# Performance work log

Hardware: AMD Instinct MI355X
Metric: run time of the kernel (lower is better)

## Reference

```python
import jax, jax.numpy as jnp
import numpy as np

N_NODES = 100000
N_EDGES = 1000000
N_GRAPHS = 64
NODE_IN = 4
HID = 64
SIG = 16
NEG_SLOPE = 0.2


def _gat_layer(x, src, dst, W, a_src, a_dst, bias, n_nodes, concat):
    # W: [H*D, F_in], a_src/a_dst: [H, D], bias: [H*D] or [D]
    H, D = a_src.shape
    h = (x @ W.T).reshape(-1, H, D)                      # [N, H, D]
    alpha_src = jnp.sum(h * a_src[None], axis=-1)        # [N, H]
    alpha_dst = jnp.sum(h * a_dst[None], axis=-1)        # [N, H]
    e = alpha_src[src] + alpha_dst[dst]                  # [E, H]
    e = jax.nn.leaky_relu(e, NEG_SLOPE)
    # segment softmax over edges grouped by destination node
    e_max = jax.ops.segment_max(e, dst, num_segments=n_nodes)   # [N, H]
    e_exp = jnp.exp(e - e_max[dst])                              # [E, H]
    denom = jax.ops.segment_sum(e_exp, dst, num_segments=n_nodes)
    alpha = e_exp / denom[dst]                                   # [E, H]
    out = jax.ops.segment_sum(alpha[:, :, None] * h[src], dst, num_segments=n_nodes)  # [N,H,D]
    if concat:
        out = out.reshape(-1, H * D)
    else:
        out = out.mean(axis=1)
    return out + bias


def setup_inputs() -> dict:
    key = jax.random.key(0)
    ks = jax.random.split(key, 16)
    x = jax.random.normal(ks[0], (N_NODES, NODE_IN), dtype=jnp.float32)
    edge_index = jax.random.randint(ks[1], (2, N_EDGES), 0, N_NODES, dtype=jnp.int32)
    batch = jnp.sort(jax.random.randint(ks[2], (N_NODES,), 0, N_GRAPHS, dtype=jnp.int32))
    s = 0.1
    # conv1: heads=2, concat -> out 128
    w1 = jax.random.normal(ks[3], (2 * HID, NODE_IN), dtype=jnp.float32) * s
    att_src1 = jax.random.normal(ks[4], (2, HID), dtype=jnp.float32) * s
    att_dst1 = jax.random.normal(ks[5], (2, HID), dtype=jnp.float32) * s
    b1 = jnp.zeros((2 * HID,), dtype=jnp.float32)
    # conv2: heads=1, mean -> out 64
    w2 = jax.random.normal(ks[6], (HID, 2 * HID), dtype=jnp.float32) * s
    att_src2 = jax.random.normal(ks[7], (1, HID), dtype=jnp.float32) * s
    att_dst2 = jax.random.normal(ks[8], (1, HID), dtype=jnp.float32) * s
    b2 = jnp.zeros((HID,), dtype=jnp.float32)
    wp = jax.random.normal(ks[9], (SIG, HID), dtype=jnp.float32) * s
    bp = jnp.zeros((SIG,), dtype=jnp.float32)
    return {"x": x, "edge_index": edge_index, "batch": batch,
            "w1": w1, "att_src1": att_src1, "att_dst1": att_dst1, "b1": b1,
            "w2": w2, "att_src2": att_src2, "att_dst2": att_dst2, "b2": b2,
            "wp": wp, "bp": bp}


def reference(x, edge_index, batch, w1, att_src1, att_dst1, b1,
              w2, att_src2, att_dst2, b2, wp, bp):
    n = x.shape[0]
    loops = jnp.arange(n, dtype=edge_index.dtype)
    src = jnp.concatenate([edge_index[0], loops])  # PyG GATConv adds self-loops
    dst = jnp.concatenate([edge_index[1], loops])
    h = jax.nn.elu(_gat_layer(x, src, dst, w1, att_src1, att_dst1, b1, n, concat=True))
    h = jax.nn.elu(_gat_layer(h, src, dst, w2, att_src2, att_dst2, b2, n, concat=False))
    # global mean pool by graph id
    sums = jax.ops.segment_sum(h, batch, num_segments=N_GRAPHS)
    cnts = jax.ops.segment_sum(jnp.ones((n,), h.dtype), batch, num_segments=N_GRAPHS)
    pooled = sums / jnp.maximum(cnts, 1.0)[:, None]
    return (pooled @ wp.T + bp).squeeze()
```

## Files before the change

### kernel.cpp

```cpp
#include <hip/hip_runtime.h>
#include <hip/hip_fp16.h>

#define N_NODES  100000
#define N_EDGES  1000000
#define E_TOT    1100000
#define E_CAP    1500000
#define N_GRAPHS 64

typedef _Float16 half8 __attribute__((ext_vector_type(8)));
typedef float    f32x4 __attribute__((ext_vector_type(4)));

__device__ __forceinline__ float elu_f(float v) {
    return v > 0.f ? v : expm1f(v);
}

__device__ __forceinline__ float lrelu(float v) {
    return v > 0.f ? v : 0.2f * v;
}

__global__ void k_pre(const float* __restrict__ w1,
                      const float* __restrict__ as1v, const float* __restrict__ ad1v,
                      const float* __restrict__ w2,
                      const float* __restrict__ as2v, const float* __restrict__ ad2v,
                      float* __restrict__ A1, float* __restrict__ D1,
                      float* __restrict__ B2, float* __restrict__ E2)
{
    int t = threadIdx.x;
    if (t < 128) {
        float acc = 0.f;
        for (int d = 0; d < 64; ++d) acc += w2[d * 128 + t] * as2v[d];
        B2[t] = acc;
    } else {
        int k = t - 128;
        float acc = 0.f;
        for (int d = 0; d < 64; ++d) acc += w2[d * 128 + k] * ad2v[d];
        E2[k] = acc;
    }
    if (t < 8) {
        int h = t >> 2, k = t & 3;
        float acc = 0.f;
        for (int d = 0; d < 64; ++d) acc += w1[(h * 64 + d) * 4 + k] * as1v[h * 64 + d];
        A1[t] = acc;
    } else if (t < 16) {
        int i = t - 8, h = i >> 2, k = i & 3;
        float acc = 0.f;
        for (int d = 0; d < 64; ++d) acc += w1[(h * 64 + d) * 4 + k] * ad1v[h * 64 + d];
        D1[i] = acc;
    }
}

__global__ void k_pre2(const float* __restrict__ w2, __half* __restrict__ w2frag)
{
    int f = blockIdx.x * 256 + threadIdx.x;
    int j = f & 7, ln = (f >> 3) & 63, g = f >> 9;
    int nt = g >> 2, ks = g & 3;
    int col = nt * 16 + (ln & 15);
    int k   = ks * 32 + ((ln >> 4) << 3) + j;
    w2frag[f] = __float2half(w2[col * 128 + k]);
}

__global__ void k_count(const int* __restrict__ ei, int* __restrict__ deg, int* __restrict__ pos)
{
    int e = blockIdx.x * blockDim.x + threadIdx.x;
    if (e >= E_TOT) return;
    int dst = (e < N_EDGES) ? ei[N_EDGES + e] : (e - N_EDGES);
    pos[e] = atomicAdd(&deg[dst], 1);
}

__global__ void k_scan1(const int* __restrict__ deg, int* __restrict__ rowptr, int* __restrict__ bsum)
{
    __shared__ int sh[256];
    int tid = threadIdx.x;
    int i = blockIdx.x * 256 + tid;
    int v = (i <= N_NODES) ? ((deg[i] + 3) & ~3) : 0;
    int acc = v;
    sh[tid] = acc; __syncthreads();
    for (int off = 1; off < 256; off <<= 1) {
        int add = (tid >= off) ? sh[tid - off] : 0;
        __syncthreads();
        acc += add;
        sh[tid] = acc;
        __syncthreads();
    }
    if (i <= N_NODES) rowptr[i] = acc - v;
    if (tid == 255) bsum[blockIdx.x] = acc;
}

__global__ void k_scan2(int* __restrict__ bsum, int nb)
{
    __shared__ int sh[512];
    int tid = threadIdx.x;
    int v = (tid < nb) ? bsum[tid] : 0;
    int acc = v;
    sh[tid] = acc; __syncthreads();
    for (int off = 1; off < 512; off <<= 1) {
        int add = (tid >= off) ? sh[tid - off] : 0;
        __syncthreads();
        acc += add;
        sh[tid] = acc;
        __syncthreads();
    }
    if (tid < nb) bsum[tid] = acc - v;
}

__global__ void k_scan3(int* __restrict__ rowptr, const int* __restrict__ bsum)
{
    int i = blockIdx.x * 256 + threadIdx.x;
    if (i <= N_NODES) rowptr[i] += bsum[blockIdx.x];
}

__global__ void k_scatter(const int* __restrict__ ei, const int* __restrict__ rowptr,
                          const int* __restrict__ pos, int* __restrict__ srcs)
{
    int e = blockIdx.x * blockDim.x + threadIdx.x;
    if (e >= E_TOT) return;
    int src = (e < N_EDGES) ? ei[e] : (e - N_EDGES);
    int dst = (e < N_EDGES) ? ei[N_EDGES + e] : (e - N_EDGES);
    srcs[rowptr[dst] + pos[e]] = src;
}

__global__ void __launch_bounds__(256) k_gather1x(
    const int* __restrict__ srcs, const int* __restrict__ rowptr, const int* __restrict__ deg,
    const float* __restrict__ x,
    const float* __restrict__ A1c, const float* __restrict__ D1c,
    float4* __restrict__ agg0, float4* __restrict__ agg1, float2* __restrict__ wsA)
{
    const int tid  = threadIdx.x;
    const int n    = blockIdx.x * 16 + (tid >> 4);
    const int lane = tid & 15;
    if (n >= N_NODES) return;

    const float4 A0 = ((const float4*)A1c)[0], A1v = ((const float4*)A1c)[1];
    const float4 D0 = ((const float4*)D1c)[0], D1v = ((const float4*)D1c)[1];
    const float4 xn = ((const float4*)x)[n];
    const float ad0 = xn.x * D0.x + xn.y * D0.y + xn.z * D0.z + xn.w * D0.w;
    const float ad1 = xn.x * D1v.x + xn.y * D1v.y + xn.z * D1v.z + xn.w * D1v.w;

    const int beg = rowptr[n], rend = beg + deg[n];
    float4 acc0 = {0.f, 0.f, 0.f, 0.f}, acc1 = {0.f, 0.f, 0.f, 0.f};
    float ws0 = 0.f, ws1 = 0.f;
    for (int j = beg + lane; j < rend; j += 16) {
        const int s = srcs[j];
        const float4 xs = ((const float4*)x)[s];
        const float as0 = xs.x * A0.x + xs.y * A0.y + xs.z * A0.z + xs.w * A0.w;
        const float as1 = xs.x * A1v.x + xs.y * A1v.y + xs.z * A1v.z + xs.w * A1v.w;
        const float w0 = __expf(lrelu(as0 + ad0));
        const float w1 = __expf(lrelu(as1 + ad1));
        acc0.x = fmaf(w0, xs.x, acc0.x); acc0.y = fmaf(w0, xs.y, acc0.y);
        acc0.z = fmaf(w0, xs.z, acc0.z); acc0.w = fmaf(w0, xs.w, acc0.w);
        acc1.x = fmaf(w1, xs.x, acc1.x); acc1.y = fmaf(w1, xs.y, acc1.y);
        acc1.z = fmaf(w1, xs.z, acc1.z); acc1.w = fmaf(w1, xs.w, acc1.w);
        ws0 += w0; ws1 += w1;
    }
    #pragma unroll
    for (int off = 1; off < 16; off <<= 1) {
        acc0.x += __shfl_xor(acc0.x, off, 64);
        acc0.y += __shfl_xor(acc0.y, off, 64);
        acc0.z += __shfl_xor(acc0.z, off, 64);
        acc0.w += __shfl_xor(acc0.w, off, 64);
        acc1.x += __shfl_xor(acc1.x, off, 64);
        acc1.y += __shfl_xor(acc1.y, off, 64);
        acc1.z += __shfl_xor(acc1.z, off, 64);
        acc1.w += __shfl_xor(acc1.w, off, 64);
        ws0    += __shfl_xor(ws0,    off, 64);
        ws1    += __shfl_xor(ws1,    off, 64);
    }
    if (lane == 0) {
        agg0[n] = acc0;
        agg1[n] = acc1;
        wsA[n]  = make_float2(ws0, ws1);
    }
}

#define H2_NPB 64
#define SROW_H_LD 136
__global__ void __launch_bounds__(256) k_h2f(
    const float4* __restrict__ agg0, const float4* __restrict__ agg1,
    const float2* __restrict__ wsA,
    const float* __restrict__ w1, const float* __restrict__ b1,
    const __half* __restrict__ w2frag,
    const float* __restrict__ B2, const float* __restrict__ E2,
    __half* __restrict__ h2h, float* __restrict__ as2, float* __restrict__ ad2)
{
    __shared__ __align__(16) _Float16 srow[H2_NPB * SROW_H_LD];
    const int tid = threadIdx.x;
    const int bn  = blockIdx.x * H2_NPB;

    #pragma unroll 4
    for (int t = 0; t < 16; ++t) {
        int i = tid + t * 256;
        int r = i >> 6, c2 = i & 63;
        int n = bn + r;
        int head = c2 >> 5;
        float4 a; float ws;
        if (n < N_NODES) {
            a = head ? agg1[n] : agg0[n];
            float2 w = wsA[n];
            ws = head ? w.y : w.x;
        } else { a = make_float4(0.f, 0.f, 0.f, 0.f); ws = 1.f; }
        const float4 wA = ((const float4*)w1)[2 * c2];
        const float4 wB = ((const float4*)w1)[2 * c2 + 1];
        const float2 bb = ((const float2*)b1)[c2];
        float inv = 1.f / ws;
        float v0 = elu_f((a.x * wA.x + a.y * wA.y + a.z * wA.z + a.w * wA.w) * inv + bb.x);
        float v1 = elu_f((a.x * wB.x + a.y * wB.y + a.z * wB.z + a.w * wB.w) * inv + bb.y);
        *(__half2*)&srow[r * SROW_H_LD + 2 * c2] = __floats2half2_rn(v0, v1);
    }
    __syncthreads();

    {
        int r = tid >> 2, q = tid & 3;
        const __half2* row = (const __half2*)&srow[r * SROW_H_LD];
        float ps = 0.f, pd = 0.f;
        #pragma unroll 4
        for (int i = 0; i < 16; ++i) {
            int c2 = q * 16 + i;
            float2 v  = __half22float2(row[c2]);
            float2 Bv = ((const float2*)B2)[c2];
            float2 Ev = ((const float2*)E2)[c2];
            ps += v.x * Bv.x + v.y * Bv.y;
            pd += v.x * Ev.x + v.y * Ev.y;
        }
        ps += __shfl_xor(ps, 1, 64); ps += __shfl_xor(ps, 2, 64);
        pd += __shfl_xor(pd, 1, 64); pd += __shfl_xor(pd, 2, 64);
        int n = bn + r;
        if (q == 0 && n < N_NODES) { as2[n] = ps; ad2[n] = pd; }
    }

    const int lane = tid & 63;
    const int wv   = tid >> 6;
    const int mrow = lane & 15;
    const int kc   = lane >> 4;
    f32x4 acc[4] = {{0.f,0.f,0.f,0.f},{0.f,0.f,0.f,0.f},{0.f,0.f,0.f,0.f},{0.f,0.f,0.f,0.f}};
    const half8* __restrict__ wf = (const half8*)w2frag;
    #pragma unroll
    for (int ks = 0; ks < 4; ++ks) {
        const half8 af = *(const half8*)&srow[(wv * 16 + mrow) * SROW_H_LD + ks * 32 + kc * 8];
        #pragma unroll
        for (int nt = 0; nt < 4; ++nt) {
            const half8 bf = wf[(nt * 4 + ks) * 64 + lane];
            acc[nt] = __builtin_amdgcn_mfma_f32_16x16x32_f16(af, bf, acc[nt], 0, 0, 0);
        }
    }
    #pragma unroll
    for (int nt = 0; nt < 4; ++nt) {
        #pragma unroll
        for (int reg = 0; reg < 4; ++reg) {
            int node = bn + wv * 16 + ((lane >> 4) << 2) + reg;
            int dim  = nt * 16 + (lane & 15);
            if (node < N_NODES) h2h[(size_t)node * 64 + dim] = __float2half(acc[nt][reg]);
        }
    }
}

__global__ void __launch_bounds__(256) k_weights2(
    const int* __restrict__ rowptr, const int* __restrict__ deg, int* __restrict__ srcs,
    const float* __restrict__ as2, const float* __restrict__ ad2,
    float* __restrict__ w0p)
{
    int n = blockIdx.x * 16 + (threadIdx.x >> 4);
    int lane = threadIdx.x & 15;
    if (n >= N_NODES) return;
    int beg = rowptr[n], pend = rowptr[n + 1], rend = beg + deg[n];
    float adv = ad2[n];
    for (int j = beg + lane; j < pend; j += 16) {
        if (j < rend) {
            w0p[j] = __expf(lrelu(as2[srcs[j]] + adv));
        } else {
            srcs[j] = 0;
            w0p[j] = 0.f;
        }
    }
}

__global__ void __launch_bounds__(256) k_gather2(
    const int* __restrict__ srcs, const int* __restrict__ rowptr,
    const float* __restrict__ wcsr, const __half2* __restrict__ h2v,
    const float* __restrict__ b2, float* __restrict__ out2)
{
    const int tid  = threadIdx.x;
    const int n    = blockIdx.x * 4 + (tid >> 6);
    const int lane = tid & 63;
    const int eh   = lane >> 5;
    const int d2   = lane & 31;
    if (n >= N_NODES) return;
    const int beg = rowptr[n], end = rowptr[n + 1];

    float2 acc = {0.f, 0.f};
    float wsum = 0.f;
    for (int j = beg; j < end; j += 4) {
        const int4   s4 = *(const int4*)(srcs + j);
        const float4 w4 = *(const float4*)(wcsr + j);
        const int   sA = eh ? s4.z : s4.x;
        const int   sB = eh ? s4.w : s4.y;
        const float wA = eh ? w4.z : w4.x;
        const float wB = eh ? w4.w : w4.y;
        const float2 vA = __half22float2(h2v[(size_t)sA * 32 + d2]);
        const float2 vB = __half22float2(h2v[(size_t)sB * 32 + d2]);
        acc.x = fmaf(wA, vA.x, acc.x); acc.y = fmaf(wA, vA.y, acc.y);
        acc.x = fmaf(wB, vB.x, acc.x); acc.y = fmaf(wB, vB.y, acc.y);
        wsum += wA + wB;
    }
    acc.x += __shfl_xor(acc.x, 32, 64);
    acc.y += __shfl_xor(acc.y, 32, 64);
    wsum  += __shfl_xor(wsum,  32, 64);
    if (eh == 0) {
        const float2 bb = ((const float2*)b2)[d2];
        float2 o;
        o.x = elu_f(acc.x / wsum + bb.x);
        o.y = elu_f(acc.y / wsum + bb.y);
        ((float2*)out2)[(size_t)n * 32 + d2] = o;
    }
}

__global__ void __launch_bounds__(256) k_pool(
    const float* __restrict__ out2, const int* __restrict__ batch,
    float* __restrict__ pool, float* __restrict__ cnt)
{
    const int wv = threadIdx.x >> 6, d = threadIdx.x & 63;
    const int wid = blockIdx.x * 4 + wv;
    const int per = (N_NODES + 2047) / 2048;
    int n0 = wid * per, n1 = min(n0 + per, N_NODES);
    if (n0 >= n1) return;
    float acc = 0.f; int g = batch[n0]; int run = 0;
    for (int n = n0; n < n1; ++n) {
        int gn = batch[n];
        if (gn != g) {
            atomicAdd(&pool[g * 64 + d], acc);
            if (d == 0) atomicAdd(&cnt[g], (float)run);
            acc = 0.f; run = 0; g = gn;
        }
        acc += out2[(size_t)n * 64 + d];
        ++run;
    }
    atomicAdd(&pool[g * 64 + d], acc);
    if (d == 0) atomicAdd(&cnt[g], (float)run);
}

__global__ void k_head(const float* __restrict__ pool, const float* __restrict__ cnt,
                       const float* __restrict__ wp, const float* __restrict__ bp,
                       float* __restrict__ out)
{
    int t = threadIdx.x;
    int g = t >> 4, s = t & 15;
    float c = cnt[g]; if (c < 1.f) c = 1.f;
    float acc = bp[s];
    for (int d = 0; d < 64; ++d) acc += (pool[g * 64 + d] / c) * wp[s * 64 + d];
    out[g * 16 + s] = acc;
}

extern "C" void kernel_launch(void* const* d_in, const int* in_sizes, int n_in,
                              void* d_out, int out_size, void* d_ws, size_t ws_size,
                              hipStream_t stream)
{
    const float* x     = (const float*)d_in[0];
    const int*   ei    = (const int*)  d_in[1];
    const int*   batch = (const int*)  d_in[2];
    const float* w1    = (const float*)d_in[3];
    const float* asr1  = (const float*)d_in[4];
    const float* adr1  = (const float*)d_in[5];
    const float* b1    = (const float*)d_in[6];
    const float* w2    = (const float*)d_in[7];
    const float* asr2  = (const float*)d_in[8];
    const float* adr2  = (const float*)d_in[9];
    const float* b2    = (const float*)d_in[10];
    const float* wp    = (const float*)d_in[11];
    const float* bp    = (const float*)d_in[12];
    float* out = (float*)d_out;

    float4* agg0 = (float4*)d_ws;
    float4* agg1 = agg0 + N_NODES;
    float2* wsA  = (float2*)(agg1 + N_NODES);
    __half* h2h  = (__half*)(wsA + N_NODES);
    float* out2  = (float*)(h2h + (size_t)N_NODES * 64);
    float* as2   = out2 + (size_t)N_NODES * 64;
    float* ad2   = as2 + N_NODES;
    float* pool  = ad2 + N_NODES;
    float* cnt   = pool + N_GRAPHS * 64;
    int* deg     = (int*)(cnt + N_GRAPHS);
    int* rowptr  = deg + N_NODES + 1;
    int* pos     = rowptr + N_NODES + 1;
    int* srcs    = pos + E_TOT;
    float* wcsr  = (float*)(srcs + E_CAP);
    int* bsum    = (int*)(wcsr + E_CAP);
    float* A1    = (float*)(bsum + 512);
    float* D1    = A1 + 8;
    float* B2    = D1 + 8;
    float* E2    = B2 + 128;
    __half* w2frag = (__half*)(((uintptr_t)(E2 + 128) + 15) & ~(uintptr_t)15);

    hipMemsetAsync(deg, 0, (size_t)(N_NODES + 1) * sizeof(int), stream);
    hipMemsetAsync(pool, 0, (size_t)(N_GRAPHS * 64 + N_GRAPHS) * sizeof(float), stream);

    k_pre<<<1, 256, 0, stream>>>(w1, asr1, adr1, w2, asr2, adr2, A1, D1, B2, E2);
    k_pre2<<<32, 256, 0, stream>>>(w2, w2frag);

    const int eb  = (E_TOT + 255) / 256;
    const int nb1 = (N_NODES + 1 + 255) / 256;
    k_count<<<eb, 256, 0, stream>>>(ei, deg, pos);
    k_scan1<<<nb1, 256, 0, stream>>>(deg, rowptr, bsum);
    k_scan2<<<1, 512, 0, stream>>>(bsum, nb1);
    k_scan3<<<nb1, 256, 0, stream>>>(rowptr, bsum);
    k_scatter<<<eb, 256, 0, stream>>>(ei, rowptr, pos, srcs);

    const int gb = (N_NODES + 15) / 16;
    k_gather1x<<<gb, 256, 0, stream>>>(srcs, rowptr, deg, x, A1, D1, agg0, agg1, wsA);

    k_h2f<<<(N_NODES + H2_NPB - 1) / H2_NPB, 256, 0, stream>>>(
        agg0, agg1, wsA, w1, b1, w2frag, B2, E2, h2h, as2, ad2);

    k_weights2<<<gb, 256, 0, stream>>>(rowptr, deg, srcs, as2, ad2, wcsr);
    k_gather2<<<(N_NODES + 3) / 4, 256, 0, stream>>>(srcs, rowptr, wcsr, (const __half2*)h2h,
                                                     b2, out2);

    k_pool<<<512, 256, 0, stream>>>(out2, batch, pool, cnt);
    k_head<<<1, 1024, 0, stream>>>(pool, cnt, wp, bp, out);
}
```

Baseline: 233.3 us.

## Gather layer-2 features with 8-edge-parallel half8 loads per node

The layer-2 gather kernel now splits each 64-lane wavefront into 8 edge groups of 8 lanes, each lane loading a 16-byte half8 chunk of a source row, then reduces across groups with shuffles. This replaces the old scheme of 2 edge halves with half2 loads, aiming for more memory-level parallelism and wider loads per gathered row. CSR row padding is raised from multiples of 4 to multiples of 8, with a larger edge capacity, so padded slots keep zero weights. The cost is more padded edges to process and a deeper shuffle reduction. The bounds check is removed, which is safe because the node count is divisible by 4.

```diff
diff --git a/kernel.cpp b/kernel.cpp
--- a/kernel.cpp
+++ b/kernel.cpp
@@ -4,7 +4,7 @@
 #define N_NODES  100000
 #define N_EDGES  1000000
 #define E_TOT    1100000
-#define E_CAP    1500000
+#define E_CAP    1900000
 #define N_GRAPHS 64
 
 typedef _Float16 half8 __attribute__((ext_vector_type(8)));
@@ -72,7 +72,7 @@
     __shared__ int sh[256];
     int tid = threadIdx.x;
     int i = blockIdx.x * 256 + tid;
-    int v = (i <= N_NODES) ? ((deg[i] + 3) & ~3) : 0;
+    int v = (i <= N_NODES) ? ((deg[i] + 7) & ~7) : 0;
     int acc = v;
     sh[tid] = acc; __syncthreads();
     for (int off = 1; off < 256; off <<= 1) {
@@ -275,41 +275,60 @@
 
 __global__ void __launch_bounds__(256) k_gather2(
     const int* __restrict__ srcs, const int* __restrict__ rowptr,
-    const float* __restrict__ wcsr, const __half2* __restrict__ h2v,
+    const float* __restrict__ wcsr, const _Float16* __restrict__ h2h,
     const float* __restrict__ b2, float* __restrict__ out2)
 {
     const int tid  = threadIdx.x;
     const int n    = blockIdx.x * 4 + (tid >> 6);
     const int lane = tid & 63;
-    const int eh   = lane >> 5;
-    const int d2   = lane & 31;
-    if (n >= N_NODES) return;
+    const int eg   = lane >> 3;
+    const int dq   = lane & 7;
     const int beg = rowptr[n], end = rowptr[n + 1];
 
-    float2 acc = {0.f, 0.f};
+    float a0=0.f,a1=0.f,a2=0.f,a3=0.f,a4=0.f,a5=0.f,a6=0.f,a7=0.f;
     float wsum = 0.f;
-    for (int j = beg; j < end; j += 4) {
-        const int4   s4 = *(const int4*)(srcs + j);
-        const float4 w4 = *(const float4*)(wcsr + j);
-        const int   sA = eh ? s4.z : s4.x;
-        const int   sB = eh ? s4.w : s4.y;
-        const float wA = eh ? w4.z : w4.x;
-        const float wB = eh ? w4.w : w4.y;
-        const float2 vA = __half22float2(h2v[(size_t)sA * 32 + d2]);
-        const float2 vB = __half22float2(h2v[(size_t)sB * 32 + d2]);
-        acc.x = fmaf(wA, vA.x, acc.x); acc.y = fmaf(wA, vA.y, acc.y);
-        acc.x = fmaf(wB, vB.x, acc.x); acc.y = fmaf(wB, vB.y, acc.y);
-        wsum += wA + wB;
-    }
-    acc.x += __shfl_xor(acc.x, 32, 64);
-    acc.y += __shfl_xor(acc.y, 32, 64);
-    wsum  += __shfl_xor(wsum,  32, 64);
-    if (eh == 0) {
-        const float2 bb = ((const float2*)b2)[d2];
-        float2 o;
-        o.x = elu_f(acc.x / wsum + bb.x);
-        o.y = elu_f(acc.y / wsum + bb.y);
-        ((float2*)out2)[(size_t)n * 32 + d2] = o;
+    for (int j = beg + eg; j < end; j += 8) {
+        const int   s = srcs[j];
+        const float w = wcsr[j];
+        const half8 v = *(const half8*)&h2h[(size_t)s * 64 + dq * 8];
+        a0 = fmaf(w, (float)v[0], a0);
+        a1 = fmaf(w, (float)v[1], a1);
+        a2 = fmaf(w, (float)v[2], a2);
+        a3 = fmaf(w, (float)v[3], a3);
+        a4 = fmaf(w, (float)v[4], a4);
+        a5 = fmaf(w, (float)v[5], a5);
+        a6 = fmaf(w, (float)v[6], a6);
+        a7 = fmaf(w, (float)v[7], a7);
+        wsum += w;
+    }
+    #pragma unroll
+    for (int off = 8; off < 64; off <<= 1) {
+        a0 += __shfl_xor(a0, off, 64);
+        a1 += __shfl_xor(a1, off, 64);
+        a2 += __shfl_xor(a2, off, 64);
+        a3 += __shfl_xor(a3, off, 64);
+        a4 += __shfl_xor(a4, off, 64);
+        a5 += __shfl_xor(a5, off, 64);
+        a6 += __shfl_xor(a6, off, 64);
+        a7 += __shfl_xor(a7, off, 64);
+        wsum += __shfl_xor(wsum, off, 64);
+    }
+    if (eg == 0) {
+        const float inv = 1.f / wsum;
+        const float4 bA = ((const float4*)b2)[dq * 2];
+        const float4 bB = ((const float4*)b2)[dq * 2 + 1];
+        float4 oA, oB;
+        oA.x = elu_f(a0 * inv + bA.x);
+        oA.y = elu_f(a1 * inv + bA.y);
+        oA.z = elu_f(a2 * inv + bA.z);
+        oA.w = elu_f(a3 * inv + bA.w);
+        oB.x = elu_f(a4 * inv + bB.x);
+        oB.y = elu_f(a5 * inv + bB.y);
+        oB.z = elu_f(a6 * inv + bB.z);
+        oB.w = elu_f(a7 * inv + bB.w);
+        float4* orow = (float4*)(out2 + (size_t)n * 64);
+        orow[dq * 2]     = oA;
+        orow[dq * 2 + 1] = oB;
     }
 }
 
@@ -410,8 +429,8 @@
         agg0, agg1, wsA, w1, b1, w2frag, B2, E2, h2h, as2, ad2);
 
     k_weights2<<<gb, 256, 0, stream>>>(rowptr, deg, srcs, as2, ad2, wcsr);
-    k_gather2<<<(N_NODES + 3) / 4, 256, 0, stream>>>(srcs, rowptr, wcsr, (const __half2*)h2h,
-                                                     b2, out2);
+    k_gather2<<<N_NODES / 4, 256, 0, stream>>>(srcs, rowptr, wcsr, (const _Float16*)h2h,
+                                               b2, out2);
 
     k_pool<<<512, 256, 0, stream>>>(out2, batch, pool, cnt);
     k_head<<<1, 1024, 0, stream>>>(pool, cnt, wp, bp, out);
```

Measured after the change: 232.4 us. About the same (-0.4%).
